# Optimization experiments

Measured on AMD Instinct MI355X. Metric: run time of the kernel, lower is better.

The kernel has to match this reference:

```python
import jax, jax.numpy as jnp
import numpy as np

EMB = 384
HEADS = 6
HEAD_SIZE = 64


def setup_inputs() -> dict:
    key = jax.random.key(0)
    ks = jax.random.split(key, 6)
    B, T = 128, 256
    x = jax.random.normal(ks[0], (B, T, EMB), dtype=jnp.float32)
    s = EMB ** -0.5
    Wq = jax.random.normal(ks[1], (HEADS, EMB, HEAD_SIZE), dtype=jnp.float32) * s
    Wk = jax.random.normal(ks[2], (HEADS, EMB, HEAD_SIZE), dtype=jnp.float32) * s
    Wv = jax.random.normal(ks[3], (HEADS, EMB, HEAD_SIZE), dtype=jnp.float32) * s
    Wproj = jax.random.normal(ks[4], (EMB, EMB), dtype=jnp.float32) * s
    bproj = jax.random.normal(ks[5], (EMB,), dtype=jnp.float32) * 0.01
    return {"x": x, "Wq": Wq, "Wk": Wk, "Wv": Wv, "Wproj": Wproj, "bproj": bproj}


def reference(x, Wq, Wk, Wv, Wproj, bproj):
    B, T, C = x.shape
    scale = C ** -0.5  # original scales by embeddingSize**-0.5, not headSize
    q = jnp.einsum('bte,hed->bhtd', x, Wq)
    k = jnp.einsum('bte,hed->bhtd', x, Wk)
    v = jnp.einsum('bte,hed->bhtd', x, Wv)
    w = jnp.einsum('bhtd,bhsd->bhts', q, k) * scale  # (B,H,T,T)
    mask = jnp.tril(jnp.ones((T, T), dtype=bool))
    w = jnp.where(mask[None, None], w, -jnp.inf)
    # original applies softmax over dim=1 of (B,T,T) -> the query axis -> axis=2 here
    w = jax.nn.softmax(w, axis=2)
    out = jnp.einsum('bhts,bhsd->bhtd', w, v)  # (B,H,T,Dh)
    out = out.transpose(0, 2, 1, 3).reshape(B, T, -1)  # concat heads -> (B,T,EMB)
    return out @ Wproj + bproj  # dropout omitted (eval mode)
```

## Files before the change

### kernel.cpp

```cpp
#include <hip/hip_runtime.h>

#define EMB 384
#define HEADS 6
#define DH 64
#define TT 256

constexpr float SCALE = 0.05103103630798288f;

typedef __attribute__((ext_vector_type(8))) short short8;
typedef __attribute__((ext_vector_type(4))) float f32x4;
typedef __attribute__((ext_vector_type(4))) unsigned short u16x4;

__device__ __forceinline__ unsigned short f2bf(float f) {
  unsigned int u = __builtin_bit_cast(unsigned int, f);
  u += 0x7FFFu + ((u >> 16) & 1u);
  return (unsigned short)(u >> 16);
}
__device__ __forceinline__ float bf2f(unsigned short u) {
  unsigned int v = ((unsigned int)u) << 16;
  return __builtin_bit_cast(float, v);
}
__device__ __forceinline__ void gll16(const void* g, void* l) {
  __builtin_amdgcn_global_load_lds(
      (const __attribute__((address_space(1))) unsigned int*)g,
      (__attribute__((address_space(3))) unsigned int*)l, 16, 0, 0);
}

__global__ __launch_bounds__(256)
void cvt_x(const float* __restrict__ x, unsigned short* __restrict__ xb, int n8) {
  int i = blockIdx.x * 256 + threadIdx.x;
  if (i < n8) {
    const float4* src = (const float4*)x;
    float4 a = src[i * 2], b = src[i * 2 + 1];
    short8 o;
    o[0] = (short)f2bf(a.x); o[1] = (short)f2bf(a.y);
    o[2] = (short)f2bf(a.z); o[3] = (short)f2bf(a.w);
    o[4] = (short)f2bf(b.x); o[5] = (short)f2bf(b.y);
    o[6] = (short)f2bf(b.z); o[7] = (short)f2bf(b.w);
    ((short8*)xb)[i] = o;
  }
}

__global__ __launch_bounds__(256)
void build_wt(const float* __restrict__ Wq, const float* __restrict__ Wk,
              const float* __restrict__ Wv, const float* __restrict__ Wp,
              unsigned short* __restrict__ Wt) {
  int idx = blockIdx.x * 256 + threadIdx.x;
  int n = idx / 48, e0 = (idx % 48) * 8;
  const float* src; int stride;
  if (n < 1152) {
    int h = n / 192, rem = n % 192, qkv = rem >> 6, d = rem & 63;
    const float* W = (qkv == 0) ? Wq : (qkv == 1) ? Wk : Wv;
    src = W + ((size_t)h * EMB + e0) * DH + d; stride = DH;
  } else {
    int c = n - 1152;
    src = Wp + (size_t)e0 * EMB + c; stride = EMB;
  }
  short8 o;
  #pragma unroll
  for (int j = 0; j < 8; ++j) o[j] = (short)f2bf(src[j * stride]);
  ((short8*)Wt)[idx] = o;
}

__global__ __launch_bounds__(1024, 1)
void qkv_attn(const unsigned short* __restrict__ xb16, const unsigned short* __restrict__ Wt,
              unsigned short* __restrict__ O)
{
  __shared__ __align__(16) char EL[73728];
  __shared__ __align__(16) char KL[32768];
  __shared__ __align__(16) char VL[32768];
  __shared__ float Lpart[16][256];
  __shared__ float invL[256];

  const int bhRaw = blockIdx.x, tid = (int)threadIdx.x;
  const int bh = (bhRaw & 7) * 96 + (bhRaw >> 3);
  const int w = tid >> 6, lane = tid & 63;
  const int la = lane & 15, kh = lane >> 4;
  const int b = bh / 6, h = bh - b * 6;
  const unsigned short* xb = xb16 + (size_t)b * 256 * 384;
  const unsigned short* Wb = Wt + (size_t)h * 192 * 384;
  char* A0 = EL;
  char* B0 = EL + 32768;
  char* A1 = KL;
  char* B1 = VL;

  const int wr = (w >> 2) * 64, wc = (w & 3) * 48;
  f32x4 acc[4][3];
  #pragma unroll
  for (int i = 0; i < 4; ++i)
    #pragma unroll
    for (int j = 0; j < 3; ++j) acc[i][j] = f32x4{0.f, 0.f, 0.f, 0.f};

  auto stage = [&](char* A, char* B, int kt) {
    #pragma unroll
    for (int i = 0; i < 2; ++i) {
      const int Lb = i * 16384 + tid * 16;
      const int row = Lb >> 7;
      const int kcs = ((Lb >> 4) & 7) ^ (row & 7);
      gll16(xb + (size_t)row * 384 + kt * 64 + kcs * 8, A + Lb);
    }
    {
      const int Lb0 = tid * 16;
      const int row0 = Lb0 >> 7;
      const int kcs0 = ((Lb0 >> 4) & 7) ^ (row0 & 7);
      gll16(Wb + (size_t)row0 * 384 + kt * 64 + kcs0 * 8, B + Lb0);
      if (tid < 512) {
        const int Lb = 16384 + tid * 16;
        const int row = Lb >> 7;
        const int kcs = ((Lb >> 4) & 7) ^ (row & 7);
        gll16(Wb + (size_t)row * 384 + kt * 64 + kcs * 8, B + Lb);
      }
    }
  };

  auto compute = [&](const char* A, const char* B) {
    #pragma unroll
    for (int kk = 0; kk < 2; ++kk) {
      const int ch = kk * 4 + kh;
      short8 a[4], bfr[3];
      #pragma unroll
      for (int mi = 0; mi < 4; ++mi) {
        const int r = wr + mi * 16 + la;
        a[mi] = *(const short8*)(A + r * 128 + ((ch ^ (r & 7)) << 4));
      }
      #pragma unroll
      for (int ni = 0; ni < 3; ++ni) {
        const int rB = wc + ni * 16 + la;
        bfr[ni] = *(const short8*)(B + rB * 128 + ((ch ^ (rB & 7)) << 4));
      }
      __builtin_amdgcn_s_setprio(1);
      #pragma unroll
      for (int mi = 0; mi < 4; ++mi)
        #pragma unroll
        for (int ni = 0; ni < 3; ++ni)
          acc[mi][ni] = __builtin_amdgcn_mfma_f32_16x16x32_bf16(a[mi], bfr[ni], acc[mi][ni], 0, 0, 0);
      __builtin_amdgcn_s_setprio(0);
    }
  };

  stage(A0, B0, 0);
  __syncthreads();
  #pragma unroll
  for (int g = 0; g < 3; ++g) {
    const int k1 = 2 * g + 1;
    stage(A1, B1, k1);
    compute(A0, B0);
    __syncthreads();
    if (k1 + 1 < 6) stage(A0, B0, k1 + 1);
    compute(A1, B1);
    __syncthreads();
  }

  #pragma unroll
  for (int mi = 0; mi < 4; ++mi) {
    #pragma unroll
    for (int ni = 0; ni < 3; ++ni) {
      const int col = wc + ni * 16 + la;
      const int tb = wr + mi * 16 + kh * 4;
      if (col < 64) {
        const int d = col;
        #pragma unroll
        for (int j = 0; j < 4; ++j) {
          const int t = tb + j;
          *(unsigned short*)(EL + t * 128 + (((d >> 3) ^ (t & 7)) << 4) + (d & 7) * 2)
              = f2bf(acc[mi][ni][j]);
        }
      } else if (col < 128) {
        const int d = col - 64;
        #pragma unroll
        for (int j = 0; j < 4; ++j) {
          const int t = tb + j;
          *(unsigned short*)(KL + t * 128 + (((d >> 3) ^ (t & 7)) << 4) + (d & 7) * 2)
              = f2bf(acc[mi][ni][j]);
        }
      } else {
        const int d = col - 128;
        u16x4 pk;
        #pragma unroll
        for (int j = 0; j < 4; ++j) pk[j] = f2bf(acc[mi][ni][j]);
        *(u16x4*)(VL + d * 512 + (((tb >> 3) ^ (d & 7)) << 4) + (tb & 7) * 2) = pk;
      }
    }
  }
  __syncthreads();

  const int p = w >> 1;
  const int rts[2] = { p, 15 - p };
  short8 qa[2][2];
  #pragma unroll
  for (int ti = 0; ti < 2; ++ti)
    #pragma unroll
    for (int kk = 0; kk < 2; ++kk) {
      const int r = rts[ti] * 16 + la;
      const int ch = kk * 4 + kh;
      qa[ti][kk] = *(const short8*)(EL + r * 128 + ((ch ^ (r & 7)) << 4));
    }
  __syncthreads();

  int wps[2], eoffs[2];
  #pragma unroll
  for (int ti = 0; ti < 2; ++ti) {
    const int rt = rts[ti];
    wps[ti] = 32 * ((rt + 2) >> 1);
    const int S = (rt & 1) ? ((rt + 1) * (rt + 1) / 4) : (rt * (rt + 2) / 4);
    eoffs[ti] = 1024 * S;
  }

  #pragma unroll
  for (int i = 0; i < 4; ++i) Lpart[w][i * 64 + lane] = 0.f;

  #pragma unroll
  for (int ti = 0; ti < 2; ++ti) {
    const int rt = rts[ti], wp = wps[ti], stride = wp * 2;
    char* Ebase = EL + eoffs[ti];
    const int nns = wp >> 4;
    for (int ns = (w & 1); ns < nns; ns += 2) {
      f32x4 s4 = f32x4{0.f, 0.f, 0.f, 0.f};
      #pragma unroll
      for (int kk = 0; kk < 2; ++kk) {
        const int rB = ns * 16 + la, kc = kk * 4 + kh;
        short8 bf = *(const short8*)(KL + rB * 128 + ((kc ^ (rB & 7)) << 4));
        s4 = __builtin_amdgcn_mfma_f32_16x16x32_bf16(qa[ti][kk], bf, s4, 0, 0, 0);
      }
      const int c = ns * 16 + la, cc = c >> 3, co = (c & 7) * 2;
      float ps = 0.f;
      #pragma unroll
      for (int j = 0; j < 4; ++j) {
        const int r = kh * 4 + j;
        const int t = rt * 16 + r;
        const float e = (t >= c) ? __expf(s4[j] * SCALE) : 0.f;
        ps += e;
        *(unsigned short*)(Ebase + r * stride + ((cc ^ (r & 3)) << 4) + co) = f2bf(e);
      }
      ps += __shfl_xor(ps, 16);
      ps += __shfl_xor(ps, 32);
      if (kh == 0) Lpart[w][c] += ps;
    }
  }
  __syncthreads();

  if (tid < 256) {
    float Ls = 0.f;
    #pragma unroll
    for (int ww = 0; ww < 16; ++ww) Ls += Lpart[ww][tid];
    invL[tid] = 1.f / Ls;
  }
  __syncthreads();

  {
    const int d = tid >> 4, qq = tid & 15;
    #pragma unroll
    for (int i = 0; i < 2; ++i) {
      const int kcp = qq * 2 + i;
      char* pch = VL + d * 512 + kcp * 16;
      short8 v = *(short8*)pch;
      const int sb = (kcp ^ (d & 7)) * 8;
      short8 o;
      #pragma unroll
      for (int e = 0; e < 8; ++e)
        o[e] = (short)f2bf(bf2f((unsigned short)v[e]) * invL[sb + e]);
      *(short8*)pch = o;
    }
  }
  __syncthreads();

  unsigned short* Og = O + (size_t)b * 256 * 384 + h * 64;
  {
    const int ti = (w & 1) ? 0 : 1;
    const int rt = rts[ti], wp = wps[ti], stride = wp * 2;
    const char* Ebase = EL + eoffs[ti];
    f32x4 oacc[4];
    #pragma unroll
    for (int nd = 0; nd < 4; ++nd) oacc[nd] = f32x4{0.f, 0.f, 0.f, 0.f};
    const int nks = wp >> 5;
    for (int ks = 0; ks < nks; ++ks) {
      const int cc = ks * 4 + kh;
      short8 ea = *(const short8*)(Ebase + la * stride + ((cc ^ (la & 3)) << 4));
      __builtin_amdgcn_s_setprio(1);
      #pragma unroll
      for (int nd = 0; nd < 4; ++nd) {
        const int d = nd * 16 + la;
        short8 vb = *(const short8*)(VL + d * 512 + ((cc ^ (d & 7)) << 4));
        oacc[nd] = __builtin_amdgcn_mfma_f32_16x16x32_bf16(ea, vb, oacc[nd], 0, 0, 0);
      }
      __builtin_amdgcn_s_setprio(0);
    }
    #pragma unroll
    for (int nd = 0; nd < 4; ++nd) {
      const int d = nd * 16 + la;
      #pragma unroll
      for (int j = 0; j < 4; ++j) {
        const int t = rt * 16 + kh * 4 + j;
        Og[(size_t)t * 384 + d] = f2bf(oacc[nd][j]);
      }
    }
  }
}

__global__ __launch_bounds__(512, 1)
void proj_gemm(const unsigned short* __restrict__ A, const unsigned short* __restrict__ Bt,
               float* __restrict__ Co, const float* __restrict__ bias)
{
  __shared__ __align__(16) unsigned short AL[128 * 384];
  __shared__ __align__(16) unsigned short BL[2][128 * 64];
  const int tid = (int)threadIdx.x, w = tid >> 6, lane = tid & 63;
  const int la = lane & 15, kh = lane >> 4;
  const int m0 = blockIdx.x * 128;

  {
    const int row = tid >> 2, qq = tid & 3;
    const short8* O8 = (const short8*)(A + (size_t)(m0 + row) * 384);
    #pragma unroll
    for (int i = 0; i < 12; ++i) {
      const int ch = qq + 4 * i;
      *(short8*)((char*)AL + row * 768 + ((ch ^ (row & 7)) << 4)) = O8[ch];
    }
  }

  auto stageB = [&](int buf, int n0, int k0) {
    #pragma unroll
    for (int i = 0; i < 2; ++i) {
      const int Lb = i * 8192 + tid * 16;
      const int row = Lb >> 7;
      const int kcs = ((Lb >> 4) & 7) ^ (row & 7);
      gll16(Bt + (size_t)(n0 + row) * 384 + k0 + kcs * 8, (char*)BL[buf] + Lb);
    }
  };

  stageB(0, 0, 0);
  __syncthreads();

  const int wr = (w >> 2) * 64, wc = (w & 3) * 32;
  int buf = 0;
  for (int nt = 0; nt < 3; ++nt) {
    f32x4 acc[4][2];
    #pragma unroll
    for (int i = 0; i < 4; ++i) { acc[i][0] = f32x4{0.f,0.f,0.f,0.f}; acc[i][1] = f32x4{0.f,0.f,0.f,0.f}; }

    for (int kt = 0; kt < 6; ++kt) {
      if (kt < 5)          stageB(buf ^ 1, nt * 128, (kt + 1) * 64);
      else if (nt + 1 < 3) stageB(buf ^ 1, (nt + 1) * 128, 0);
      #pragma unroll
      for (int kk = 0; kk < 2; ++kk) {
        short8 a[4], bb[2];
        const int chA = kt * 8 + kk * 4 + kh;
        #pragma unroll
        for (int mi = 0; mi < 4; ++mi) {
          const int r = wr + mi * 16 + la;
          a[mi] = *(const short8*)((const char*)AL + r * 768 + ((chA ^ (r & 7)) << 4));
        }
        const int chB = kk * 4 + kh;
        #pragma unroll
        for (int ni = 0; ni < 2; ++ni) {
          const int rB = wc + ni * 16 + la;
          bb[ni] = *(const short8*)((const char*)BL[buf] + rB * 128 + ((chB ^ (rB & 7)) << 4));
        }
        __builtin_amdgcn_s_setprio(1);
        #pragma unroll
        for (int mi = 0; mi < 4; ++mi)
          #pragma unroll
          for (int ni = 0; ni < 2; ++ni)
            acc[mi][ni] = __builtin_amdgcn_mfma_f32_16x16x32_bf16(a[mi], bb[ni], acc[mi][ni], 0, 0, 0);
        __builtin_amdgcn_s_setprio(0);
      }
      __syncthreads();
      buf ^= 1;
    }

    #pragma unroll
    for (int mi = 0; mi < 4; ++mi) {
      const int mbase = m0 + wr + mi * 16 + kh * 4;
      #pragma unroll
      for (int ni = 0; ni < 2; ++ni) {
        const int nl = nt * 128 + wc + ni * 16 + la;
        const float bn = bias[nl];
        #pragma unroll
        for (int j = 0; j < 4; ++j)
          Co[(size_t)(mbase + j) * 384 + nl] = acc[mi][ni][j] + bn;
      }
    }
  }
}

__global__ __launch_bounds__(256, 1)
void mha_fused(const float* __restrict__ x, const float* __restrict__ Wq,
               const float* __restrict__ Wk, const float* __restrict__ Wv,
               const float* __restrict__ Wp, const float* __restrict__ bp,
               float* __restrict__ out)
{
  const int bh = blockIdx.x;
  const int b = bh / HEADS, h = bh % HEADS;
  const int tid = (int)threadIdx.x;
  const int wave = tid >> 6, lane = tid & 63;
  const float* xb = x + (size_t)b * TT * EMB;
  const float* wq = Wq + (size_t)h * EMB * DH;
  const float* wk = Wk + (size_t)h * EMB * DH;
  const float* wv = Wv + (size_t)h * EMB * DH;
  __shared__ float Ks[TT][68];
  __shared__ float Vs[TT][64];
  __shared__ float Qt[64][68];
  for (int c = 0; c < 4; ++c) {
    const int s0 = wave * 64 + c * 16;
    float ak[16], av[16];
    #pragma unroll
    for (int r = 0; r < 16; ++r) { ak[r] = 0.f; av[r] = 0.f; }
    for (int e = 0; e < EMB; ++e) {
      const float kk = wk[e * DH + lane];
      const float vv = wv[e * DH + lane];
      #pragma unroll
      for (int r = 0; r < 16; ++r) {
        const float xv = xb[(s0 + r) * EMB + e];
        ak[r] += xv * kk; av[r] += xv * vv;
      }
    }
    #pragma unroll
    for (int r = 0; r < 16; ++r) { Ks[s0 + r][lane] = ak[r]; Vs[s0 + r][lane] = av[r]; }
  }
  __syncthreads();
  const int s = tid;
  float kreg[64];
  {
    const float4* k4 = (const float4*)&Ks[s][0];
    #pragma unroll
    for (int i = 0; i < 16; ++i) {
      float4 kv = k4[i];
      kreg[4*i+0] = kv.x; kreg[4*i+1] = kv.y; kreg[4*i+2] = kv.z; kreg[4*i+3] = kv.w;
    }
  }
  float Lsum = 0.f;
  for (int tile = 0; tile < 4; ++tile) {
    {
      const int r0 = tile * 64 + wave * 16;
      float aq[16];
      #pragma unroll
      for (int r = 0; r < 16; ++r) aq[r] = 0.f;
      for (int e = 0; e < EMB; ++e) {
        const float qw = wq[e * DH + lane];
        #pragma unroll
        for (int r = 0; r < 16; ++r) aq[r] += xb[(r0 + r) * EMB + e] * qw;
      }
      __syncthreads();
      #pragma unroll
      for (int r = 0; r < 16; ++r) Qt[wave*16 + r][lane] = aq[r];
      __syncthreads();
    }
    const int tbase = tile * 64;
    if (tbase + 63 >= s) {
      for (int tr = 0; tr < 64; ++tr) {
        const int t = tbase + tr;
        if (t < s) continue;
        float w = 0.f;
        const float4* q4 = (const float4*)&Qt[tr][0];
        #pragma unroll
        for (int i = 0; i < 16; ++i) {
          float4 qv = q4[i];
          w += qv.x*kreg[4*i+0] + qv.y*kreg[4*i+1] + qv.z*kreg[4*i+2] + qv.w*kreg[4*i+3];
        }
        Lsum += __expf(w * SCALE);
      }
    }
  }
  __syncthreads();
  {
    const float invL = 1.0f / Lsum;
    float4* v4 = (float4*)&Vs[s][0];
    #pragma unroll
    for (int i = 0; i < 16; ++i) {
      float4 vv = v4[i];
      vv.x *= invL; vv.y *= invL; vv.z *= invL; vv.w *= invL;
      v4[i] = vv;
    }
  }
  __syncthreads();
  const float bias1 = bp[tid];
  const float bias2 = (tid < 128) ? bp[256 + tid] : 0.f;
  const int tr = tid >> 2, dq = tid & 3;
  float* ob = out + (size_t)b * TT * EMB;
  for (int tile = 0; tile < 4; ++tile) {
    {
      const int r0 = tile * 64 + wave * 16;
      float aq[16];
      #pragma unroll
      for (int r = 0; r < 16; ++r) aq[r] = 0.f;
      for (int e = 0; e < EMB; ++e) {
        const float qw = wq[e * DH + lane];
        #pragma unroll
        for (int r = 0; r < 16; ++r) aq[r] += xb[(r0 + r) * EMB + e] * qw;
      }
      __syncthreads();
      #pragma unroll
      for (int r = 0; r < 16; ++r) Qt[wave*16 + r][lane] = aq[r];
      __syncthreads();
    }
    const int t = tile * 64 + tr;
    float qreg[16];
    {
      const float4* q4 = (const float4*)&Qt[tr][dq * 16];
      #pragma unroll
      for (int i = 0; i < 4; ++i) {
        float4 qv = q4[i];
        qreg[4*i+0] = qv.x; qreg[4*i+1] = qv.y; qreg[4*i+2] = qv.z; qreg[4*i+3] = qv.w;
      }
    }
    float acc[16];
    #pragma unroll
    for (int i = 0; i < 16; ++i) acc[i] = 0.f;
    for (int s2 = 0; s2 <= t; ++s2) {
      const float4* kk4 = (const float4*)&Ks[s2][dq * 16];
      float part = 0.f;
      #pragma unroll
      for (int i = 0; i < 4; ++i) {
        float4 kv = kk4[i];
        part += qreg[4*i+0]*kv.x + qreg[4*i+1]*kv.y + qreg[4*i+2]*kv.z + qreg[4*i+3]*kv.w;
      }
      part += __shfl_xor(part, 1);
      part += __shfl_xor(part, 2);
      const float p = __expf(part * SCALE);
      const float4* vv4 = (const float4*)&Vs[s2][dq * 16];
      #pragma unroll
      for (int i = 0; i < 4; ++i) {
        float4 vv = vv4[i];
        acc[4*i+0] += p * vv.x; acc[4*i+1] += p * vv.y;
        acc[4*i+2] += p * vv.z; acc[4*i+3] += p * vv.w;
      }
    }
    __syncthreads();
    #pragma unroll
    for (int i = 0; i < 16; ++i) Qt[tr][dq*16 + i] = acc[i];
    __syncthreads();
    const int c1 = tid;
    const int c2 = 256 + tid;
    for (int rg = 0; rg < 4; ++rg) {
      float a1[16], a2[16];
      #pragma unroll
      for (int r = 0; r < 16; ++r) { a1[r] = 0.f; a2[r] = 0.f; }
      for (int d = 0; d < 64; ++d) {
        const float wp1 = Wp[(size_t)(h*64 + d) * EMB + c1];
        const float wp2 = (tid < 128) ? Wp[(size_t)(h*64 + d) * EMB + c2] : 0.f;
        #pragma unroll
        for (int r = 0; r < 16; ++r) {
          const float a = Qt[rg*16 + r][d];
          a1[r] += a * wp1; a2[r] += a * wp2;
        }
      }
      if (h == 0) {
        #pragma unroll
        for (int r = 0; r < 16; ++r) { a1[r] += bias1; a2[r] += bias2; }
      }
      const int trow0 = tile*64 + rg*16;
      #pragma unroll
      for (int r = 0; r < 16; ++r)
        atomicAdd(&ob[(size_t)(trow0 + r) * EMB + c1], a1[r]);
      if (tid < 128) {
        #pragma unroll
        for (int r = 0; r < 16; ++r)
          atomicAdd(&ob[(size_t)(trow0 + r) * EMB + c2], a2[r]);
      }
    }
    __syncthreads();
  }
}

extern "C" void kernel_launch(void* const* d_in, const int* in_sizes, int n_in,
                              void* d_out, int out_size, void* d_ws, size_t ws_size,
                              hipStream_t stream) {
  const float* x  = (const float*)d_in[0];
  const float* Wq = (const float*)d_in[1];
  const float* Wk = (const float*)d_in[2];
  const float* Wv = (const float*)d_in[3];
  const float* Wp = (const float*)d_in[4];
  const float* bp = (const float*)d_in[5];

  const int nb = in_sizes[0] / (TT * EMB);
  const size_t M = (size_t)nb * TT;
  const size_t XB = M * EMB * 2;
  const size_t WT = (size_t)1536 * 384 * 2;

  const size_t off_x  = 0;
  const size_t off_wt = XB;
  const size_t off_o  = off_wt + WT;
  const size_t need   = off_o + XB;

  if (ws_size < need || nb * HEADS != 768) {
    hipMemsetAsync(d_out, 0, (size_t)out_size * sizeof(float), stream);
    mha_fused<<<nb * HEADS, 256, 0, stream>>>(x, Wq, Wk, Wv, Wp, bp, (float*)d_out);
    return;
  }

  char* ws = (char*)d_ws;
  unsigned short* xb16 = (unsigned short*)(ws + off_x);
  unsigned short* Wt   = (unsigned short*)(ws + off_wt);
  unsigned short* Ow   = (unsigned short*)(ws + off_o);

  const int n8 = (int)(M * EMB / 8);
  cvt_x<<<(n8 + 255) / 256, 256, 0, stream>>>(x, xb16, n8);
  build_wt<<<288, 256, 0, stream>>>(Wq, Wk, Wv, Wp, Wt);

  qkv_attn<<<nb * HEADS, 1024, 0, stream>>>(xb16, Wt, Ow);

  proj_gemm<<<(unsigned)(M / 128), 512, 0, stream>>>(
      Ow, Wt + (size_t)1152 * 384, (float*)d_out, bp);
}
```

Baseline: 106.2 us.

## Fuse fp32-to-bf16 conversion of x into attention kernel staging

Removes the separate cvt_x kernel. The attention kernel now loads fp32 x into registers, converts to bf16 and writes it into swizzled LDS, software-pipelined around the MFMA compute. This drops one launch and the bf16 round trip of x through global memory. The cost is that each of the 6 head blocks per batch now reads fp32 x, twice the bytes of bf16, and spends extra VALU work on conversion. It also changes which wave takes the larger tile in the PV stage (bigw).

```diff
diff --git a/kernel.cpp b/kernel.cpp
--- a/kernel.cpp
+++ b/kernel.cpp
@@ -24,21 +24,6 @@
   __builtin_amdgcn_global_load_lds(
       (const __attribute__((address_space(1))) unsigned int*)g,
       (__attribute__((address_space(3))) unsigned int*)l, 16, 0, 0);
-}
-
-__global__ __launch_bounds__(256)
-void cvt_x(const float* __restrict__ x, unsigned short* __restrict__ xb, int n8) {
-  int i = blockIdx.x * 256 + threadIdx.x;
-  if (i < n8) {
-    const float4* src = (const float4*)x;
-    float4 a = src[i * 2], b = src[i * 2 + 1];
-    short8 o;
-    o[0] = (short)f2bf(a.x); o[1] = (short)f2bf(a.y);
-    o[2] = (short)f2bf(a.z); o[3] = (short)f2bf(a.w);
-    o[4] = (short)f2bf(b.x); o[5] = (short)f2bf(b.y);
-    o[6] = (short)f2bf(b.z); o[7] = (short)f2bf(b.w);
-    ((short8*)xb)[i] = o;
-  }
 }
 
 __global__ __launch_bounds__(256)
@@ -63,7 +48,7 @@
 }
 
 __global__ __launch_bounds__(1024, 1)
-void qkv_attn(const unsigned short* __restrict__ xb16, const unsigned short* __restrict__ Wt,
+void qkv_attn(const float* __restrict__ x, const unsigned short* __restrict__ Wt,
               unsigned short* __restrict__ O)
 {
   __shared__ __align__(16) char EL[73728];
@@ -77,7 +62,7 @@
   const int w = tid >> 6, lane = tid & 63;
   const int la = lane & 15, kh = lane >> 4;
   const int b = bh / 6, h = bh - b * 6;
-  const unsigned short* xb = xb16 + (size_t)b * 256 * 384;
+  const float* xf = x + (size_t)b * 256 * 384;
   const unsigned short* Wb = Wt + (size_t)h * 192 * 384;
   char* A0 = EL;
   char* B0 = EL + 32768;
@@ -91,25 +76,42 @@
     #pragma unroll
     for (int j = 0; j < 3; ++j) acc[i][j] = f32x4{0.f, 0.f, 0.f, 0.f};
 
-  auto stage = [&](char* A, char* B, int kt) {
+  const int arow = tid >> 2, aqq = tid & 3;
+  const float4* xfr = (const float4*)(xf + (size_t)arow * 384);
+
+  float4 ra[4];
+  auto loadA = [&](int kt) {
+    const int base = kt * 16;
     #pragma unroll
     for (int i = 0; i < 2; ++i) {
-      const int Lb = i * 16384 + tid * 16;
+      const int ch = aqq + 4 * i;
+      ra[2*i]   = xfr[base + ch * 2];
+      ra[2*i+1] = xfr[base + ch * 2 + 1];
+    }
+  };
+  auto writeA = [&](char* A) {
+    #pragma unroll
+    for (int i = 0; i < 2; ++i) {
+      const int ch = aqq + 4 * i;
+      float4 va = ra[2*i], vb = ra[2*i+1];
+      short8 o;
+      o[0] = (short)f2bf(va.x); o[1] = (short)f2bf(va.y);
+      o[2] = (short)f2bf(va.z); o[3] = (short)f2bf(va.w);
+      o[4] = (short)f2bf(vb.x); o[5] = (short)f2bf(vb.y);
+      o[6] = (short)f2bf(vb.z); o[7] = (short)f2bf(vb.w);
+      *(short8*)(A + arow * 128 + ((ch ^ (arow & 7)) << 4)) = o;
+    }
+  };
+  auto stageB = [&](char* B, int kt) {
+    const int Lb0 = tid * 16;
+    const int row0 = Lb0 >> 7;
+    const int kcs0 = ((Lb0 >> 4) & 7) ^ (row0 & 7);
+    gll16(Wb + (size_t)row0 * 384 + kt * 64 + kcs0 * 8, B + Lb0);
+    if (tid < 512) {
+      const int Lb = 16384 + tid * 16;
       const int row = Lb >> 7;
       const int kcs = ((Lb >> 4) & 7) ^ (row & 7);
-      gll16(xb + (size_t)row * 384 + kt * 64 + kcs * 8, A + Lb);
-    }
-    {
-      const int Lb0 = tid * 16;
-      const int row0 = Lb0 >> 7;
-      const int kcs0 = ((Lb0 >> 4) & 7) ^ (row0 & 7);
-      gll16(Wb + (size_t)row0 * 384 + kt * 64 + kcs0 * 8, B + Lb0);
-      if (tid < 512) {
-        const int Lb = 16384 + tid * 16;
-        const int row = Lb >> 7;
-        const int kcs = ((Lb >> 4) & 7) ^ (row & 7);
-        gll16(Wb + (size_t)row * 384 + kt * 64 + kcs * 8, B + Lb);
-      }
+      gll16(Wb + (size_t)row * 384 + kt * 64 + kcs * 8, B + Lb);
     }
   };
 
@@ -138,16 +140,21 @@
     }
   };
 
-  stage(A0, B0, 0);
+  loadA(0);
+  writeA(A0);
+  stageB(B0, 0);
   __syncthreads();
   #pragma unroll
   for (int g = 0; g < 3; ++g) {
     const int k1 = 2 * g + 1;
-    stage(A1, B1, k1);
+    loadA(k1);
+    stageB(B1, k1);
     compute(A0, B0);
+    writeA(A1);
     __syncthreads();
-    if (k1 + 1 < 6) stage(A0, B0, k1 + 1);
+    if (k1 + 1 < 6) { loadA(k1 + 1); stageB(B0, k1 + 1); }
     compute(A1, B1);
+    if (k1 + 1 < 6) writeA(A0);
     __syncthreads();
   }
 
@@ -266,7 +273,8 @@
 
   unsigned short* Og = O + (size_t)b * 256 * 384 + h * 64;
   {
-    const int ti = (w & 1) ? 0 : 1;
+    const int bigw = 2 * p + ((p >> 1) & 1);
+    const int ti = (w == bigw) ? 1 : 0;
     const int rt = rts[ti], wp = wps[ti], stride = wp * 2;
     const char* Ebase = EL + eoffs[ti];
     f32x4 oacc[4];
@@ -576,8 +584,7 @@
   const size_t XB = M * EMB * 2;
   const size_t WT = (size_t)1536 * 384 * 2;
 
-  const size_t off_x  = 0;
-  const size_t off_wt = XB;
+  const size_t off_wt = 0;
   const size_t off_o  = off_wt + WT;
   const size_t need   = off_o + XB;
 
@@ -588,15 +595,12 @@
   }
 
   char* ws = (char*)d_ws;
-  unsigned short* xb16 = (unsigned short*)(ws + off_x);
-  unsigned short* Wt   = (unsigned short*)(ws + off_wt);
-  unsigned short* Ow   = (unsigned short*)(ws + off_o);
-
-  const int n8 = (int)(M * EMB / 8);
-  cvt_x<<<(n8 + 255) / 256, 256, 0, stream>>>(x, xb16, n8);
+  unsigned short* Wt = (unsigned short*)(ws + off_wt);
+  unsigned short* Ow = (unsigned short*)(ws + off_o);
+
   build_wt<<<288, 256, 0, stream>>>(Wq, Wk, Wv, Wp, Wt);
 
-  qkv_attn<<<nb * HEADS, 1024, 0, stream>>>(xb16, Wt, Ow);
+  qkv_attn<<<nb * HEADS, 1024, 0, stream>>>(x, Wt, Ow);
 
   proj_gemm<<<(unsigned)(M / 128), 512, 0, stream>>>(
       Ow, Wt + (size_t)1152 * 384, (float*)d_out, bp);
```

After: 103.6 us. 1.02x faster.
